# Kernel tuning notes

Hardware: AMD Instinct MI355X
Metric: run time of the kernel (lower is better)

## Reference

```python
import jax, jax.numpy as jnp
import numpy as np

B, T, C, NH = 8, 1024, 1024, 16
HD = C // NH
EPS = 1e-5


def setup_inputs() -> dict:
    key = jax.random.key(0)
    k1, k2, k3 = jax.random.split(key, 3)
    x = jax.random.normal(k1, (B, T, C), dtype=jnp.float32)
    past_kv = jax.random.normal(k2, (NH, HD, HD), dtype=jnp.float32) * 0.1
    W_qkv = jax.random.normal(k3, (C, 3 * C), dtype=jnp.float32) * 0.02
    gn_weight = jnp.ones((NH,), dtype=jnp.float32)
    gn_bias = jnp.zeros((NH,), dtype=jnp.float32)
    return {"x": x, "past_kv": past_kv, "W_qkv": W_qkv,
            "gn_weight": gn_weight, "gn_bias": gn_bias}


def _decay_mask(nh, t, dtype):
    # decay_mask[h, i, j] = gamma[h]**(i-j) if i >= j else 0
    gamma = 1.0 - 2.0 ** (-5.0 - jnp.arange(nh, dtype=jnp.float32))
    idx = jnp.arange(t)
    diff = idx[:, None] - idx[None, :]            # [T, T]
    mask = diff >= 0
    pow_ = gamma[:, None, None] ** jnp.where(mask, diff, 0).astype(jnp.float32)
    return jnp.where(mask[None], pow_, 0.0).astype(dtype), gamma.astype(dtype)


def reference(x, past_kv, W_qkv, gn_weight, gn_bias):
    b, t, c = x.shape
    nh = gn_weight.shape[0]
    hd = c // nh

    qkv = x @ W_qkv                               # [B, T, 3C]
    q, k, v = jnp.split(qkv, 3, axis=2)
    split_heads = lambda u: u.reshape(b, t, nh, hd).transpose(0, 2, 1, 3)  # [B,nh,T,hd]
    q, k, v = split_heads(q), split_heads(k), split_heads(v)

    decay, gamma = _decay_mask(nh, t, x.dtype)    # [nh,T,T], [nh]

    # intra-chunk: decay-masked QK^T @ V
    ret = jnp.einsum('bhtd,bhsd->bhts', q, k) * decay      # [B,nh,T,T]
    inner = jnp.einsum('bhts,bhsd->bhtd', ret, v)          # [B,nh,T,hd]

    # cross-chunk: q @ past_kv * (n_head * chunk_size)
    inner_decay = float(nh * hd)
    cross = jnp.einsum('bhtd,hde->bhte', q, past_kv) * inner_decay
    r = inner + cross                                      # [B,nh,T,hd]

    # recurrent state update: gamma * past_kv + k^T @ v, then mean over batch
    current_kv = gamma[:, None, None] * past_kv + jnp.einsum('bhtd,bhte->bhde', k, v)
    current_kv = current_kv.mean(axis=0)                   # [nh,hd,hd]

    # GroupNorm(1, n_head) on [B, nh, hd, T] (single group => stats over all non-batch dims)
    y = r.transpose(0, 1, 3, 2)                            # [B,nh,hd,T]
    mu = y.mean(axis=(1, 2, 3), keepdims=True)
    var = y.var(axis=(1, 2, 3), keepdims=True)             # biased, matches torch GroupNorm
    yn = (y - mu) * jax.lax.rsqrt(var + EPS)
    yn = yn * gn_weight[None, :, None, None] + gn_bias[None, :, None, None]

    # rearrange 'b c h t -> b t (c h)'
    out = yn.transpose(0, 3, 1, 2).reshape(b, t, c)
    return out, current_kv
```

## Files before the change

### kernel.cpp

```cpp
#include <hip/hip_runtime.h>


#define TKN 8192
#define N3  3072

typedef short short8 __attribute__((ext_vector_type(8)));
typedef float f32x4 __attribute__((ext_vector_type(4)));

static __device__ __forceinline__ unsigned short f2bf(float f){
  unsigned int u = __float_as_uint(f);
  u += 0x7FFFu + ((u >> 16) & 1u);
  return (unsigned short)(u >> 16);
}
static __device__ __forceinline__ float bf2f(unsigned short s){
  return __uint_as_float(((unsigned int)s) << 16);
}
static __device__ __forceinline__ void g2lds16(const void* g, void* l){
  __builtin_amdgcn_global_load_lds(
      (const __attribute__((address_space(1))) unsigned int*)g,
      (__attribute__((address_space(3))) unsigned int*)l, 16, 0, 0);
}

__global__ __launch_bounds__(256) void k_cvt(const float* __restrict__ x,
                                             const float* __restrict__ w,
                                             const float* __restrict__ pk,
                                             unsigned short* __restrict__ xb,
                                             unsigned short* __restrict__ wt,
                                             unsigned short* __restrict__ pkt){
  __shared__ float tile[64][65];
  const int bid = blockIdx.x;
  if (bid < 2048){
    const int n4 = TKN*1024/4;
    for (int idx = bid*256 + threadIdx.x; idx < n4; idx += 2048*256){
      float4 v = reinterpret_cast<const float4*>(x)[idx];
      ushort4 o;
      o.x = f2bf(v.x); o.y = f2bf(v.y); o.z = f2bf(v.z); o.w = f2bf(v.w);
      reinterpret_cast<ushort4*>(xb)[idx] = o;
    }
  } else if (bid < 2816){
    const int b2 = bid - 2048;
    const int n0 = (b2 % 48)*64, k0 = (b2 / 48)*64;
    const int tn = threadIdx.x & 63, t4 = threadIdx.x >> 6;
    for (int kk = t4; kk < 64; kk += 4)
      tile[kk][tn] = w[(k0+kk)*N3 + n0 + tn];
    __syncthreads();
    for (int nn = t4; nn < 64; nn += 4)
      wt[(n0+nn)*1024 + k0 + tn] = f2bf(tile[tn][nn]);
  } else {
    int i = (bid - 2816)*256 + threadIdx.x;
    int h = i >> 12, e = (i >> 6) & 63, d = i & 63;
    pkt[i] = f2bf(pk[(h<<12) + (d<<6) + e] * 1024.0f);
  }
}

__global__ __launch_bounds__(256, 3) void k_gemm(const unsigned short* __restrict__ A,
                                                 const unsigned short* __restrict__ Bt,
                                                 unsigned short* __restrict__ qb,
                                                 unsigned short* __restrict__ kb,
                                                 unsigned short* __restrict__ vtb){
  __shared__ unsigned short sm[24576];
  char* smb = (char*)sm;
  const int tid = threadIdx.x;
  const int lane = tid & 63, wid = tid >> 6;
  const int wm = wid >> 1, wn = wid & 1;
  const int n15 = lane & 15, l4 = lane >> 4;
  const int m0 = blockIdx.y * 128;
  const int n0 = blockIdx.x * 128;

  f32x4 acc[4][4] = {};

  const int l0 = tid >> 2;
  const int r0 = (l0 & ~3) | ((l0 & 1) << 1) | ((l0 >> 1) & 1);
  const int c0 = (((tid & 3) ^ ((tid >> 4) & 3)) << 3);
  #define STAGE(kt, b) do {                                                              \
    g2lds16(A  + (long)(m0 + r0)*1024      + (kt)*32 + c0, smb + (b)*8192 + tid*16);     \
    g2lds16(A  + (long)(m0 + 64 + r0)*1024 + (kt)*32 + c0, smb + (b)*8192 + 4096 + tid*16); \
    g2lds16(Bt + (long)(n0 + r0)*1024      + (kt)*32 + c0, smb + 24576 + (b)*8192 + tid*16); \
    g2lds16(Bt + (long)(n0 + 64 + r0)*1024 + (kt)*32 + c0, smb + 24576 + (b)*8192 + 4096 + tid*16); \
  } while(0)

  STAGE(0, 0);
  STAGE(1, 1);
  asm volatile("s_waitcnt vmcnt(4)" ::: "memory");
  __builtin_amdgcn_s_barrier();

  const int slb = (l4 ^ ((n15 >> 2) & 3)) << 4;
  int cur = 0;
  for (int t = 0; t < 32; ++t){
    int nb = cur + 2; if (nb >= 3) nb -= 3;
    if (t < 30) STAGE(t + 2, nb);
    const char* ab = smb + cur*8192;
    const char* bb = smb + 24576 + cur*8192;
    short8 a[4], b[4];
    #pragma unroll
    for (int i = 0; i < 4; ++i){
      int ra = wm*64 + i*16 + n15;
      int rs = (ra & ~3) | ((ra & 1) << 1) | ((ra >> 1) & 1);
      a[i] = *(const short8*)(ab + rs*64 + slb);
      int rb = wn*64 + i*16 + n15;
      int rbs = (rb & ~3) | ((rb & 1) << 1) | ((rb >> 1) & 1);
      b[i] = *(const short8*)(bb + rbs*64 + slb);
    }
    __builtin_amdgcn_s_setprio(1);
    #pragma unroll
    for (int i = 0; i < 4; ++i)
      #pragma unroll
      for (int j = 0; j < 4; ++j)
        acc[i][j] = __builtin_amdgcn_mfma_f32_16x16x32_bf16(a[i], b[j], acc[i][j], 0, 0, 0);
    __builtin_amdgcn_s_setprio(0);
    if (t < 30) asm volatile("s_waitcnt vmcnt(4)" ::: "memory");
    else        asm volatile("s_waitcnt vmcnt(0)" ::: "memory");
    __builtin_amdgcn_s_barrier();
    cur = cur + 1; if (cur == 3) cur = 0;
  }
  #undef STAGE

  const int bb2 = m0 >> 10;
  const int which = n0 >> 10;
  const int cw = (n0 & 1023) + wn*64;
  const int h = cw >> 6;
  const long bh = (long)(bb2*16 + h);
  const int trow0 = (m0 & 1023) + wm*64;
  char* W = smb + wid*8192;

  if (which < 2){
    unsigned short* dst = which ? kb : qb;
    #pragma unroll
    for (int mi = 0; mi < 4; ++mi)
      #pragma unroll
      for (int nf = 0; nf < 4; ++nf)
        #pragma unroll
        for (int r = 0; r < 4; ++r){
          int row = mi*16 + l4*4 + r;
          int colb = (nf*32 + 2*n15) ^ ((row & 7) << 4);
          *(unsigned short*)(W + row*128 + colb) = f2bf(acc[mi][nf][r]);
        }
    asm volatile("s_waitcnt lgkmcnt(0)" ::: "memory");
    #pragma unroll
    for (int hh = 0; hh < 2; ++hh)
      #pragma unroll
      for (int c2 = 0; c2 < 4; ++c2){
        int row = hh*32 + (lane >> 1);
        int off = ((lane & 1)*64 + c2*16) ^ ((row & 7) << 4);
        uint4 v = *(const uint4*)(W + row*128 + off);
        int dcol = (lane & 1)*32 + c2*8;
        *(uint4*)(&dst[(bh*1024 + trow0 + row)*64 + dcol]) = v;
      }
  } else {
    #pragma unroll
    for (int mi = 0; mi < 4; ++mi)
      #pragma unroll
      for (int nf = 0; nf < 4; ++nf)
        #pragma unroll
        for (int r = 0; r < 4; ++r){
          int dl = nf*16 + n15;
          int row = mi*16 + l4*4 + r;
          int colb = (2*row) ^ ((dl & 7) << 4);
          *(unsigned short*)(W + dl*128 + colb) = f2bf(acc[mi][nf][r]);
        }
    asm volatile("s_waitcnt lgkmcnt(0)" ::: "memory");
    #pragma unroll
    for (int hh = 0; hh < 2; ++hh)
      #pragma unroll
      for (int c2 = 0; c2 < 4; ++c2){
        int dl = hh*32 + (lane >> 1);
        int off = ((lane & 1)*64 + c2*16) ^ ((dl & 7) << 4);
        uint4 v = *(const uint4*)(W + dl*128 + off);
        int tcol = (lane & 1)*32 + c2*8;
        *(uint4*)(&vtb[(bh*64 + dl)*1024 + trow0 + tcol]) = v;
      }
  }
}

__global__ __launch_bounds__(256) void k_attn(const unsigned short* __restrict__ qb,
                                              const unsigned short* __restrict__ kb,
                                              const unsigned short* __restrict__ vtb,
                                              const unsigned short* __restrict__ pkt,
                                              unsigned short* __restrict__ rb,
                                              float* __restrict__ gnp){
  __shared__ unsigned short Qs[8192];
  __shared__ unsigned short Kd[2][4096];
  __shared__ unsigned short Vd[2][4096];
  __shared__ unsigned short Ps[8192];
  __shared__ float gred[2][4];
  const int id = blockIdx.x;
  const int lin = (id & 7)*64 + (id >> 3);
  const int qpair = lin & 3;
  const int bh = lin >> 2;
  const int h = bh & 15;
  const int tid = threadIdx.x;
  const int lane = tid & 63, wid = tid >> 6;
  const int n15 = lane & 15, l4 = lane >> 4;
  const unsigned short* qp = qb + (long)bh*65536;
  const unsigned short* kp = kb + (long)bh*65536;
  const unsigned short* vp = vtb + (long)bh*65536;
  const float lg = log2f(1.0f - exp2f(-5.0f - (float)h));
  const int srow = tid >> 3, schunk = tid & 7;

  char* const kb0 = (char*)Kd[0]; char* const kb1 = (char*)Kd[1]; char* const kb2 = (char*)Qs;
  char* const vb0 = (char*)Vd[0]; char* const vb1 = (char*)Vd[1]; char* const vb2 = (char*)Qs + 8192;

  float kvE[4][4];
  #pragma unroll
  for (int i = 0; i < 4; ++i)
    #pragma unroll
    for (int r = 0; r < 4; ++r)
      kvE[i][r] = exp2f(-lg * (float)(i*16 + l4*4 + r));

  float gs = 0.f, gq = 0.f;
  unsigned short* rp = rb + (long)bh*65536;

  for (int p = 0; p < 2; ++p){
    const int qt = p ? (7 - qpair) : qpair;
    const int t0 = qt * 128;
    const int jmax = 2*qt + 1;
    for (int c = 0; c < 4; ++c){
      int r = c*32 + srow;
      int src = schunk ^ (r & 7);
      g2lds16(qp + (long)(t0 + r)*64 + src*8, (char*)Qs + c*4096 + tid*16);
    }
    for (int c = 0; c < 2; ++c){
      int r = c*32 + srow;
      int src = schunk ^ (r & 7);
      g2lds16(pkt + (long)(h*64 + r)*64 + src*8, (char*)Ps + c*4096 + tid*16);
      g2lds16(kp + (long)r*64 + src*8, kb0 + c*4096 + tid*16);
      g2lds16(vp + (long)r*1024 + src*8, vb0 + c*4096 + tid*16);
    }
    for (int c = 0; c < 2; ++c){
      int r = c*32 + srow;
      int src = schunk ^ (r & 7);
      g2lds16(kp + (long)(64 + r)*64 + src*8, kb1 + c*4096 + tid*16);
      g2lds16(vp + (long)r*1024 + 64 + src*8, vb1 + c*4096 + tid*16);
    }
    asm volatile("s_waitcnt vmcnt(4)" ::: "memory");
    __syncthreads();

    short8 aq[2][2];
    #pragma unroll
    for (int mf = 0; mf < 2; ++mf)
      #pragma unroll
      for (int kk = 0; kk < 2; ++kk){
        int r = wid*32 + mf*16 + n15;
        int sl = (kk*4 + l4) ^ (r & 7);
        aq[mf][kk] = *reinterpret_cast<const short8*>((const char*)Qs + r*128 + sl*16);
      }

    f32x4 o[2][4] = {};
    #pragma unroll
    for (int kk = 0; kk < 2; ++kk){
      short8 bpk[4];
      #pragma unroll
      for (int nf = 0; nf < 4; ++nf){
        int r = nf*16 + n15;
        int sl = (kk*4 + l4) ^ (r & 7);
        bpk[nf] = *reinterpret_cast<const short8*>((const char*)Ps + r*128 + sl*16);
      }
      #pragma unroll
      for (int mf = 0; mf < 2; ++mf)
        #pragma unroll
        for (int nf = 0; nf < 4; ++nf)
          o[mf][nf] = __builtin_amdgcn_mfma_f32_16x16x32_bf16(aq[mf][kk], bpk[nf], o[mf][nf], 0,0,0);
    }
    __syncthreads();

    int curb = 0, sjb = 2;
    for (int j = 0; j <= jmax; ++j){
      const int kv0 = j*64;
      const bool willstage = (j + 2 <= jmax);
      if (willstage){
        const int kvn = kv0 + 128;
        char* kbs = (sjb == 0) ? kb0 : ((sjb == 1) ? kb1 : kb2);
        char* vbs = (sjb == 0) ? vb0 : ((sjb == 1) ? vb1 : vb2);
        for (int c = 0; c < 2; ++c){
          int r = c*32 + srow;
          int src = schunk ^ (r & 7);
          g2lds16(kp + (long)(kvn + r)*64 + src*8, kbs + c*4096 + tid*16);
          g2lds16(vp + (long)r*1024 + kvn + src*8, vbs + c*4096 + tid*16);
        }
      }
      const bool active = (kv0 <= t0 + wid*32 + 31);
      if (active){
        const char* kcur = (curb == 0) ? kb0 : ((curb == 1) ? kb1 : kb2);
        const char* vcur = (curb == 0) ? vb0 : ((curb == 1) ? vb1 : vb2);
        f32x4 sT[4][2] = {};
        #pragma unroll
        for (int kk = 0; kk < 2; ++kk){
          short8 bk[4];
          #pragma unroll
          for (int i = 0; i < 4; ++i){
            int r = i*16 + n15;
            int sl = (kk*4 + l4) ^ (r & 7);
            bk[i] = *reinterpret_cast<const short8*>(kcur + r*128 + sl*16);
          }
          #pragma unroll
          for (int i = 0; i < 4; ++i)
            #pragma unroll
            for (int mf = 0; mf < 2; ++mf)
              sT[i][mf] = __builtin_amdgcn_mfma_f32_16x16x32_bf16(bk[i], aq[mf][kk], sT[i][mf], 0,0,0);
        }
        const bool diag = (kv0 + 63 > t0 + wid*32);
        #pragma unroll
        for (int mf = 0; mf < 2; ++mf){
          const int trow = wid*32 + mf*16 + n15;
          const float rowE = exp2f(lg * (float)(t0 + trow - kv0));
          char* wb = (char*)Ps + trow*128;
          const int swz = (trow & 7) << 4;
          #pragma unroll
          for (int i = 0; i < 4; ++i){
            float v0 = sT[i][mf][0] * (rowE * kvE[i][0]);
            float v1 = sT[i][mf][1] * (rowE * kvE[i][1]);
            float v2 = sT[i][mf][2] * (rowE * kvE[i][2]);
            float v3 = sT[i][mf][3] * (rowE * kvE[i][3]);
            if (diag){
              int dd = (t0 + trow) - (kv0 + i*16 + l4*4);
              if (dd < 0) v0 = 0.f;
              if (dd < 1) v1 = 0.f;
              if (dd < 2) v2 = 0.f;
              if (dd < 3) v3 = 0.f;
            }
            uint2 pw;
            pw.x = (unsigned int)f2bf(v0) | ((unsigned int)f2bf(v1) << 16);
            pw.y = (unsigned int)f2bf(v2) | ((unsigned int)f2bf(v3) << 16);
            *(uint2*)(wb + ((i*32 + l4*8) ^ swz)) = pw;
          }
        }
        #pragma unroll
        for (int kk = 0; kk < 2; ++kk){
          short8 ap[2], bv[4];
          #pragma unroll
          for (int mf = 0; mf < 2; ++mf){
            int r = wid*32 + mf*16 + n15;
            int sl = (kk*4 + l4) ^ (r & 7);
            ap[mf] = *reinterpret_cast<const short8*>((const char*)Ps + r*128 + sl*16);
          }
          #pragma unroll
          for (int nf = 0; nf < 4; ++nf){
            int r = nf*16 + n15;
            int sl = (kk*4 + l4) ^ (r & 7);
            bv[nf] = *reinterpret_cast<const short8*>(vcur + r*128 + sl*16);
          }
          #pragma unroll
          for (int mf = 0; mf < 2; ++mf)
            #pragma unroll
            for (int nf = 0; nf < 4; ++nf)
              o[mf][nf] = __builtin_amdgcn_mfma_f32_16x16x32_bf16(ap[mf], bv[nf], o[mf][nf], 0,0,0);
        }
      }
      if (willstage) asm volatile("s_waitcnt vmcnt(4)" ::: "memory");
      else           asm volatile("s_waitcnt vmcnt(0)" ::: "memory");
      __syncthreads();
      curb = (curb == 2) ? 0 : curb + 1;
      sjb  = (sjb  == 2) ? 0 : sjb  + 1;
    }
    #pragma unroll
    for (int mf = 0; mf < 2; ++mf)
      #pragma unroll
      for (int nf = 0; nf < 4; ++nf)
        #pragma unroll
        for (int r = 0; r < 4; ++r){
          int trow = wid*32 + mf*16 + l4*4 + r;
          int d = nf*16 + n15;
          float v = o[mf][nf][r];
          gs += v; gq += v*v;
          *(unsigned short*)((char*)Ps + trow*128 + ((2*d) ^ ((trow & 7) << 4))) = f2bf(v);
        }
    asm volatile("s_waitcnt lgkmcnt(0)" ::: "memory");
    #pragma unroll
    for (int rr = 0; rr < 4; ++rr){
      int row = wid*32 + rr*8 + (lane >> 3);
      int off = (((lane & 7) << 4) ^ ((row & 7) << 4));
      uint4 v = *(const uint4*)((const char*)Ps + row*128 + off);
      *(uint4*)(rp + (long)(t0 + row)*64 + ((lane & 7) << 3)) = v;
    }
    __syncthreads();
  }
  #pragma unroll
  for (int off = 32; off > 0; off >>= 1){
    gs += __shfl_down(gs, off);
    gq += __shfl_down(gq, off);
  }
  if (lane == 0){ gred[0][wid] = gs; gred[1][wid] = gq; }
  __syncthreads();
  if (tid == 0){
    gnp[(bh*4 + qpair)*2]   = gred[0][0]+gred[0][1]+gred[0][2]+gred[0][3];
    gnp[(bh*4 + qpair)*2+1] = gred[1][0]+gred[1][1]+gred[1][2]+gred[1][3];
  }
}

__global__ __launch_bounds__(256) void k_kvpart(const unsigned short* __restrict__ kb,
                                                const unsigned short* __restrict__ vtb,
                                                float* __restrict__ part){
  __shared__ unsigned short Kt[64*64];
  __shared__ unsigned int   Vt32[64*33];
  const int id = blockIdx.x;
  const int lin = (id & 7)*64 + (id >> 3);
  const int tc = lin & 3, bh = lin >> 2;
  const int tid = threadIdx.x;
  const int d0 = (tid >> 4) << 2;
  const int e0 = (tid & 15) << 2;
  const unsigned short* kp = kb + (long)bh*65536;
  const unsigned short* vp = vtb + (long)bh*65536;
  float acc[4][4] = {{0.f}};
  for (int tt = 0; tt < 4; ++tt){
    const int tb = tc*256 + tt*64;
    __syncthreads();
    {
      int rr0 = tid >> 3, off = (tid & 7) * 8;
      for (int c = 0; c < 2; ++c){
        int r = c*32 + rr0;
        *reinterpret_cast<uint4*>(&Kt[r*64 + off]) =
            *reinterpret_cast<const uint4*>(&kp[(long)(tb + r)*64 + off]);
        uint4 vv = *reinterpret_cast<const uint4*>(&vp[(long)r*1024 + tb + off]);
        unsigned int* dv = &Vt32[r*33 + (off >> 1)];
        dv[0] = vv.x; dv[1] = vv.y; dv[2] = vv.z; dv[3] = vv.w;
      }
    }
    __syncthreads();
    const unsigned short* Vt = (const unsigned short*)Vt32;
    for (int t = 0; t < 64; ++t){
      float kv[4], vv[4];
      #pragma unroll
      for (int i = 0; i < 4; ++i) kv[i] = bf2f(Kt[t*64 + d0 + i]);
      #pragma unroll
      for (int i = 0; i < 4; ++i) vv[i] = bf2f(Vt[(e0 + i)*66 + t]);
      #pragma unroll
      for (int i = 0; i < 4; ++i)
        #pragma unroll
        for (int j = 0; j < 4; ++j) acc[i][j] += kv[i]*vv[j];
    }
  }
  float* pp = part + ((long)(tc*128 + bh) << 12);
  for (int i = 0; i < 4; ++i)
    for (int j = 0; j < 4; ++j)
      pp[(d0+i)*64 + e0 + j] = acc[i][j];
}

__global__ __launch_bounds__(256) void k_kvfin(const float* __restrict__ part,
                                               const float* __restrict__ pk,
                                               float* __restrict__ okv,
                                               const float* __restrict__ gnp,
                                               float* __restrict__ musig){
  if (blockIdx.x == 0 && threadIdx.x < 8){
    int b = threadIdx.x;
    float S = 0.f, Q = 0.f;
    for (int g = 0; g < 64; ++g){ S += gnp[b*128 + g*2]; Q += gnp[b*128 + g*2 + 1]; }
    float mu  = S * (1.0f/1048576.0f);
    float var = Q * (1.0f/1048576.0f) - mu*mu;
    musig[b*2]   = mu;
    musig[b*2+1] = rsqrtf(var + 1e-5f);
  }
  int i = blockIdx.x*256 + threadIdx.x;
  int h = i >> 12;
  float acc = 0.f;
  for (int tc = 0; tc < 4; ++tc)
    for (int b = 0; b < 8; ++b)
      acc += part[((long)(tc*128 + b*16 + h) << 12) + (i & 4095)];
  float gamma = 1.0f - exp2f(-5.0f - (float)h);
  okv[i] = gamma * pk[i] + acc * 0.125f;
}

__global__ __launch_bounds__(256) void k_gnnorm(const unsigned short* __restrict__ rbuf,
                                                const float* __restrict__ musig,
                                                const float* __restrict__ gw,
                                                const float* __restrict__ gb,
                                                float* __restrict__ out){
  const int n8 = TKN*1024/8;
  for (int idx = blockIdx.x*256 + threadIdx.x; idx < n8; idx += gridDim.x*256){
    int o = idx*8;
    int c = o & 1023;
    int t = (o >> 10) & 1023;
    int b = o >> 20;
    int h = c >> 6, d = c & 63;
    short8 v = *reinterpret_cast<const short8*>(rbuf + ((long)(b*16 + h) << 16) + t*64 + d);
    float rs = musig[b*2+1];
    float a = gw[h]*rs, b2 = gb[h] - musig[b*2]*a;
    float4 o0, o1;
    o0.x = bf2f((unsigned short)v[0])*a + b2;
    o0.y = bf2f((unsigned short)v[1])*a + b2;
    o0.z = bf2f((unsigned short)v[2])*a + b2;
    o0.w = bf2f((unsigned short)v[3])*a + b2;
    o1.x = bf2f((unsigned short)v[4])*a + b2;
    o1.y = bf2f((unsigned short)v[5])*a + b2;
    o1.z = bf2f((unsigned short)v[6])*a + b2;
    o1.w = bf2f((unsigned short)v[7])*a + b2;
    *reinterpret_cast<float4*>(out + o)     = o0;
    *reinterpret_cast<float4*>(out + o + 4) = o1;
  }
}

extern "C" void kernel_launch(void* const* d_in, const int* in_sizes, int n_in,
                              void* d_out, int out_size, void* d_ws, size_t ws_size,
                              hipStream_t stream){
  const float* x  = (const float*)d_in[0];
  const float* pk = (const float*)d_in[1];
  const float* w  = (const float*)d_in[2];
  const float* gw = (const float*)d_in[3];
  const float* gb = (const float*)d_in[4];
  float* out = (float*)d_out;
  char* ws = (char*)d_ws;

  unsigned short* Xb  = (unsigned short*)(ws);
  unsigned short* WTb = (unsigned short*)(ws + 16777216);
  unsigned short* Qb  = (unsigned short*)(ws + 23068672);
  unsigned short* Kb  = (unsigned short*)(ws + 39845888);
  unsigned short* VTb = (unsigned short*)(ws + 56623104);
  unsigned short* PKt = (unsigned short*)(ws + 73400320);
  unsigned short* Rb  = (unsigned short*)(ws + 73531392);
  float* KVp = (float*)(ws);
  float* GNp = (float*)(ws + 90308608);
  float* MuS = (float*)(ws + 90312704);

  k_cvt    <<<dim3(3072),    dim3(256), 0, stream>>>(x, w, pk, Xb, WTb, PKt);
  k_gemm   <<<dim3(24, 64),  dim3(256), 0, stream>>>(Xb, WTb, Qb, Kb, VTb);
  k_kvpart <<<dim3(512),     dim3(256), 0, stream>>>(Kb, VTb, KVp);
  k_attn   <<<dim3(512),     dim3(256), 0, stream>>>(Qb, Kb, VTb, PKt, Rb, GNp);
  k_kvfin  <<<dim3(256),     dim3(256), 0, stream>>>(KVp, pk, out + 8388608, GNp, MuS);
  k_gnnorm <<<dim3(1024),    dim3(256), 0, stream>>>(Rb, MuS, gw, gb, out);
}
```

Before: 161.4 us.

## Compute K^T V partials with MFMA using an extra transposed K output

The GEMM epilogue now also writes K in a transposed [bh, d, t] layout, alongside the existing row-major K. The kvpart kernel drops its scalar FMA loop over LDS tiles. It instead loads K^T and V^T fragments directly from global memory and accumulates with bf16 16x16x32 MFMA, using 8 per-wave partials per (b,h). The final reduction is reindexed to match. The cost is an extra 16 MB write in the GEMM epilogue plus an additional LDS transpose pass, in exchange for a much cheaper k^T v reduction.

Measured after the change: 167.0 us. 3.5% more time.

```diff
diff --git a/kernel.cpp b/kernel.cpp
--- a/kernel.cpp
+++ b/kernel.cpp
@@ -57,6 +57,7 @@
                                                  const unsigned short* __restrict__ Bt,
                                                  unsigned short* __restrict__ qb,
                                                  unsigned short* __restrict__ kb,
+                                                 unsigned short* __restrict__ ktb,
                                                  unsigned short* __restrict__ vtb){
   __shared__ unsigned short sm[24576];
   char* smb = (char*)sm;
@@ -146,7 +147,10 @@
         int dcol = (lane & 1)*32 + c2*8;
         *(uint4*)(&dst[(bh*1024 + trow0 + row)*64 + dcol]) = v;
       }
-  } else {
+  }
+  if (which >= 1){
+    unsigned short* dst2 = (which == 1) ? ktb : vtb;
+    if (which == 1){ asm volatile("s_waitcnt lgkmcnt(0)" ::: "memory"); }
     #pragma unroll
     for (int mi = 0; mi < 4; ++mi)
       #pragma unroll
@@ -167,7 +171,7 @@
         int off = ((lane & 1)*64 + c2*16) ^ ((dl & 7) << 4);
         uint4 v = *(const uint4*)(W + dl*128 + off);
         int tcol = (lane & 1)*32 + c2*8;
-        *(uint4*)(&vtb[(bh*64 + dl)*1024 + trow0 + tcol]) = v;
+        *(uint4*)(&dst2[(bh*64 + dl)*1024 + trow0 + tcol]) = v;
       }
   }
 }
@@ -387,52 +391,40 @@
   }
 }
 
-__global__ __launch_bounds__(256) void k_kvpart(const unsigned short* __restrict__ kb,
+__global__ __launch_bounds__(256) void k_kvpart(const unsigned short* __restrict__ ktb,
                                                 const unsigned short* __restrict__ vtb,
                                                 float* __restrict__ part){
-  __shared__ unsigned short Kt[64*64];
-  __shared__ unsigned int   Vt32[64*33];
-  const int id = blockIdx.x;
-  const int lin = (id & 7)*64 + (id >> 3);
-  const int tc = lin & 3, bh = lin >> 2;
+  const int tw = blockIdx.x;
+  const int bh = blockIdx.y;
   const int tid = threadIdx.x;
-  const int d0 = (tid >> 4) << 2;
-  const int e0 = (tid & 15) << 2;
-  const unsigned short* kp = kb + (long)bh*65536;
-  const unsigned short* vp = vtb + (long)bh*65536;
-  float acc[4][4] = {{0.f}};
-  for (int tt = 0; tt < 4; ++tt){
-    const int tb = tc*256 + tt*64;
-    __syncthreads();
-    {
-      int rr0 = tid >> 3, off = (tid & 7) * 8;
-      for (int c = 0; c < 2; ++c){
-        int r = c*32 + rr0;
-        *reinterpret_cast<uint4*>(&Kt[r*64 + off]) =
-            *reinterpret_cast<const uint4*>(&kp[(long)(tb + r)*64 + off]);
-        uint4 vv = *reinterpret_cast<const uint4*>(&vp[(long)r*1024 + tb + off]);
-        unsigned int* dv = &Vt32[r*33 + (off >> 1)];
-        dv[0] = vv.x; dv[1] = vv.y; dv[2] = vv.z; dv[3] = vv.w;
-      }
-    }
-    __syncthreads();
-    const unsigned short* Vt = (const unsigned short*)Vt32;
-    for (int t = 0; t < 64; ++t){
-      float kv[4], vv[4];
-      #pragma unroll
-      for (int i = 0; i < 4; ++i) kv[i] = bf2f(Kt[t*64 + d0 + i]);
-      #pragma unroll
-      for (int i = 0; i < 4; ++i) vv[i] = bf2f(Vt[(e0 + i)*66 + t]);
-      #pragma unroll
-      for (int i = 0; i < 4; ++i)
-        #pragma unroll
-        for (int j = 0; j < 4; ++j) acc[i][j] += kv[i]*vv[j];
-    }
-  }
-  float* pp = part + ((long)(tc*128 + bh) << 12);
+  const int lane = tid & 63, wid = tid >> 6;
+  const int n15 = lane & 15, l4 = lane >> 4;
+  const unsigned short* kt = ktb + (long)bh*65536;
+  const unsigned short* vt = vtb + (long)bh*65536;
+  const int tb = tw*512 + wid*128;
+  f32x4 acc[4][4] = {};
+  for (int ks = 0; ks < 4; ++ks){
+    const int toff = tb + ks*32 + l4*8;
+    short8 a[4], b[4];
+    #pragma unroll
+    for (int i = 0; i < 4; ++i){
+      a[i] = *reinterpret_cast<const short8*>(kt + (long)(i*16 + n15)*1024 + toff);
+      b[i] = *reinterpret_cast<const short8*>(vt + (long)(i*16 + n15)*1024 + toff);
+    }
+    #pragma unroll
+    for (int i = 0; i < 4; ++i)
+      #pragma unroll
+      for (int jn = 0; jn < 4; ++jn)
+        acc[i][jn] = __builtin_amdgcn_mfma_f32_16x16x32_bf16(a[i], b[jn], acc[i][jn], 0,0,0);
+  }
+  float* pp = part + ((long)(bh*8 + tw*4 + wid) << 12);
+  #pragma unroll
   for (int i = 0; i < 4; ++i)
-    for (int j = 0; j < 4; ++j)
-      pp[(d0+i)*64 + e0 + j] = acc[i][j];
+    #pragma unroll
+    for (int jn = 0; jn < 4; ++jn)
+      #pragma unroll
+      for (int r = 0; r < 4; ++r)
+        pp[(i*16 + l4*4 + r)*64 + jn*16 + n15] = acc[i][jn][r];
 }
 
 __global__ __launch_bounds__(256) void k_kvfin(const float* __restrict__ part,
@@ -450,11 +442,13 @@
     musig[b*2+1] = rsqrtf(var + 1e-5f);
   }
   int i = blockIdx.x*256 + threadIdx.x;
-  int h = i >> 12;
+  int h = i >> 12, de = i & 4095;
   float acc = 0.f;
-  for (int tc = 0; tc < 4; ++tc)
-    for (int b = 0; b < 8; ++b)
-      acc += part[((long)(tc*128 + b*16 + h) << 12) + (i & 4095)];
+  for (int b = 0; b < 8; ++b){
+    const float* pp = part + (((long)(b*16 + h)*8) << 12) + de;
+    #pragma unroll
+    for (int w = 0; w < 8; ++w) acc += pp[w*4096];
+  }
   float gamma = 1.0f - exp2f(-5.0f - (float)h);
   okv[i] = gamma * pk[i] + acc * 0.125f;
 }
@@ -504,15 +498,16 @@
   unsigned short* Qb  = (unsigned short*)(ws + 23068672);
   unsigned short* Kb  = (unsigned short*)(ws + 39845888);
   unsigned short* VTb = (unsigned short*)(ws + 56623104);
-  unsigned short* PKt = (unsigned short*)(ws + 73400320);
-  unsigned short* Rb  = (unsigned short*)(ws + 73531392);
+  unsigned short* KTb = (unsigned short*)(ws + 73400320);
+  unsigned short* PKt = (unsigned short*)(ws + 90177536);
+  unsigned short* Rb  = (unsigned short*)(ws + 90308608);
   float* KVp = (float*)(ws);
-  float* GNp = (float*)(ws + 90308608);
-  float* MuS = (float*)(ws + 90312704);
+  float* GNp = (float*)(ws + 107085824);
+  float* MuS = (float*)(ws + 107089920);
 
   k_cvt    <<<dim3(3072),    dim3(256), 0, stream>>>(x, w, pk, Xb, WTb, PKt);
-  k_gemm   <<<dim3(24, 64),  dim3(256), 0, stream>>>(Xb, WTb, Qb, Kb, VTb);
-  k_kvpart <<<dim3(512),     dim3(256), 0, stream>>>(Kb, VTb, KVp);
+  k_gemm   <<<dim3(24, 64),  dim3(256), 0, stream>>>(Xb, WTb, Qb, Kb, KTb, VTb);
+  k_kvpart <<<dim3(2, 128),  dim3(256), 0, stream>>>(KTb, VTb, KVp);
   k_attn   <<<dim3(512),     dim3(256), 0, stream>>>(Qb, Kb, VTb, PKt, Rb, GNp);
   k_kvfin  <<<dim3(256),     dim3(256), 0, stream>>>(KVp, pk, out + 8388608, GNp, MuS);
   k_gnnorm <<<dim3(1024),    dim3(256), 0, stream>>>(Rb, MuS, gw, gb, out);
```
